# Kernel optimization log

Measured on AMD Instinct MI355X. Metric: run time of the kernel, lower is better.

The kernel has to match this reference:

```python
import jax, jax.numpy as jnp
import numpy as np

MAX_LEN = 200
MAX_K = 3
ITERATION = 3
NEG_PAD = -2.0 ** 16 + 1.0


def setup_inputs() -> dict:
    key = jax.random.key(0)
    k1, k2, k3, k4 = jax.random.split(key, 4)
    B, L, D_in, D_out = 1024, MAX_LEN, 128, 128
    low_capsule = jax.random.normal(k1, (B, L, D_in), dtype=jnp.float32)
    B_matrix = jax.random.normal(k2, (1, MAX_K, L), dtype=jnp.float32)
    S_matrix = jax.random.normal(k3, (D_in, D_out), dtype=jnp.float32)
    # lengths in [1, MAX_LEN]; at least one row hits MAX_LEN so max(seq_len)==MAX_LEN
    seq_len = jax.random.randint(k4, (B, 1), 1, MAX_LEN + 1, dtype=jnp.int64)
    seq_len = seq_len.at[0, 0].set(MAX_LEN)
    return {"low_capsule": low_capsule, "B_matrix": B_matrix,
            "S_matrix": S_matrix, "seq_len": seq_len}


def squash(x):
    # torch code: norm over dim=1 (the capsule axis), keepdim
    sq = jnp.sum(jnp.square(x), axis=1, keepdims=True)
    scale = sq / (1.0 + sq) / jnp.sqrt(sq + 1e-9)
    return scale * x


def reference(low_capsule, B_matrix, S_matrix, seq_len):
    # low_capsule: [B, L, D_in], B_matrix: [1, K, L], S_matrix: [D_in, D_out], seq_len: [B, 1]
    # mask: [B, K, L] (seq_len tiled over K via broadcasting)
    mask = jnp.arange(MAX_LEN)[None, None, :] < seq_len[:, :, None]
    # bilinear projection is loop-invariant (same math as recomputing each iter)
    low_new = jnp.einsum('bld,de->ble', low_capsule, S_matrix)  # [B, L, D_out]
    high = None
    for _ in range(ITERATION):
        logits = jnp.where(mask, B_matrix, jnp.float32(NEG_PAD))  # [B, K, L]
        W = jax.nn.softmax(logits, axis=-1)
        high = squash(jnp.einsum('bkl,ble->bke', W, low_new))  # [B, K, D_out]
        # agreement, summed over batch with keepdim -> [1, K, L]
        B_delta = jnp.einsum('bke,ble->kl', high, low_new)[None]
        B_matrix = B_matrix + B_delta
    return high
```

## Files before the change

### kernel.cpp

```cpp
#include <hip/hip_runtime.h>
#include <math.h>

#define BATCH 1024
#define SEQ   200
#define DIN   128
#define DOUT  128
#define HALF  64
#define PSTR  608

typedef __attribute__((ext_vector_type(8))) short short8;
typedef __attribute__((ext_vector_type(4))) float f32x4;

__device__ __forceinline__ void async_copy16(const void* g, void* l) {
    __builtin_amdgcn_global_load_lds((const __attribute__((address_space(1))) void*)g,
                                     (__attribute__((address_space(3))) void*)l,
                                     16, 0, 0);
}

__device__ __forceinline__ unsigned pack_split(float f) {
    unsigned u = __float_as_uint(f);
    unsigned r = u + 0x8000u;
    unsigned hi = r >> 16;
    float hf = __uint_as_float(r & 0xffff0000u);
    unsigned lo = __float_as_uint(f - hf) >> 16;
    return (hi << 16) | lo;
}

__device__ __forceinline__ void split2(float f, short& h, short& l) {
    unsigned u = __float_as_uint(f);
    unsigned r = u + 0x8000u;
    h = (short)(r >> 16);
    float hf = __uint_as_float(r & 0xffff0000u);
    l = (short)(__float_as_uint(f - hf) >> 16);
}

__device__ __forceinline__ float unpk(unsigned u) {
    return __uint_as_float(u & 0xffff0000u) + __uint_as_float(u << 16);
}

__global__ __launch_bounds__(256) void k_presplit(const float* __restrict__ S,
                                                  short* __restrict__ Sp) {
    int g = blockIdx.x * 256 + threadIdx.x;
    int j = g & 7, lane = (g >> 3) & 63, kt = (g >> 9) & 3, nt = g >> 11;
    int k = kt * 32 + (lane >> 4) * 8 + j;
    int n = nt * 16 + (lane & 15);
    short h, l;
    split2(S[k * DOUT + n], h, l);
    Sp[g] = h;
    Sp[16384 + g] = l;
}

__global__ __launch_bounds__(256, 2) void k_gemm(const float* __restrict__ A,
                                                 const short* __restrict__ Sp,
                                                 unsigned* __restrict__ outp) {
    __shared__ short sSp[32768];
    const int t = threadIdx.x;
    const int w = t >> 6, lane = t & 63;
    const int q = lane >> 4, c = lane & 15;
    const long rowb = (long)blockIdx.x * 128 + w * 32;

    float4 araw[4][2][2];
#pragma unroll
    for (int kt = 0; kt < 4; ++kt)
#pragma unroll
        for (int mt = 0; mt < 2; ++mt) {
            const float* ap = A + (rowb + mt * 16 + c) * DIN + kt * 32 + q * 8;
            araw[kt][mt][0] = *(const float4*)ap;
            araw[kt][mt][1] = *(const float4*)(ap + 4);
        }

#pragma unroll
    for (int i = 0; i < 16; ++i) {
        const int g = w * 16 + i;
        async_copy16(Sp + g * 512 + lane * 8, &sSp[g * 512]);
    }

    short8 ah[4][2], al[4][2];
#pragma unroll
    for (int kt = 0; kt < 4; ++kt)
#pragma unroll
        for (int mt = 0; mt < 2; ++mt) {
            float av[8];
            *(float4*)&av[0] = araw[kt][mt][0];
            *(float4*)&av[4] = araw[kt][mt][1];
#pragma unroll
            for (int j = 0; j < 8; ++j) {
                short h, l;
                split2(av[j], h, l);
                ah[kt][mt][j] = h; al[kt][mt][j] = l;
            }
        }

    f32x4 acc[2][8];
    const f32x4 zz = {0.f, 0.f, 0.f, 0.f};
#pragma unroll
    for (int mt = 0; mt < 2; ++mt)
#pragma unroll
        for (int nt = 0; nt < 8; ++nt) acc[mt][nt] = zz;

    __syncthreads();

#pragma unroll
    for (int kt = 0; kt < 4; ++kt)
#pragma unroll
        for (int nt = 0; nt < 8; ++nt) {
            const int fo = ((nt * 4 + kt) * 64 + lane) * 8;
            short8 sh = *(const short8*)&sSp[fo];
            short8 sl = *(const short8*)&sSp[16384 + fo];
#pragma unroll
            for (int mt = 0; mt < 2; ++mt) {
                acc[mt][nt] = __builtin_amdgcn_mfma_f32_16x16x32_bf16(ah[kt][mt], sh, acc[mt][nt], 0, 0, 0);
                acc[mt][nt] = __builtin_amdgcn_mfma_f32_16x16x32_bf16(al[kt][mt], sh, acc[mt][nt], 0, 0, 0);
                acc[mt][nt] = __builtin_amdgcn_mfma_f32_16x16x32_bf16(ah[kt][mt], sl, acc[mt][nt], 0, 0, 0);
            }
        }
#pragma unroll
    for (int mt = 0; mt < 2; ++mt)
#pragma unroll
        for (int nt = 0; nt < 8; ++nt) {
            long r0 = rowb + mt * 16 + q * 4;
#pragma unroll
            for (int r = 0; r < 4; ++r)
                outp[(r0 + r) * DOUT + nt * 16 + c] = pack_split(acc[mt][nt][r]);
        }
}

__global__ __launch_bounds__(256, 2) void k_iter(
    const unsigned* __restrict__ lowp,
    const float* __restrict__ Bm,
    const int* __restrict__ seq,
    const float* __restrict__ acc0, const float* __restrict__ acc1,
    float* __restrict__ part,
    float* __restrict__ out, int iter) {
    __shared__ unsigned sLn[SEQ * HALF];
    __shared__ float sW[SEQ * 4];
    __shared__ float pB[4][3][HALF];
    __shared__ float sH[3][HALF];

    const int t = threadIdx.x;
    const int lane = t & 63, w = t >> 6;
    const int b = blockIdx.x >> 1, half = blockIdx.x & 1;
    const unsigned* lp = lowp + (size_t)b * (SEQ * DIN) + half * HALF;
    const int n = seq[b];

    float a0v[4], a1v[4], a2v[4];
    if (w < 3) {
        const int k = w;
#pragma unroll
        for (int i = 0; i < 4; ++i) {
            int l = lane + 64 * i;
            bool inb = (l < SEQ);
            a0v[i] = inb ? Bm[k * SEQ + l] : 0.f;
            a1v[i] = (inb && iter >= 1) ? acc0[k * SEQ + l] : 0.f;
            a2v[i] = (inb && iter >= 2) ? acc1[k * SEQ + l] : 0.f;
        }
    }

    for (int g = w; g < 50; g += 4)
        async_copy16(lp + (g * 4 + (lane >> 4)) * DIN + (lane & 15) * 4,
                     &sLn[g * 256]);

    if (w < 3) {
        const int k = w;
        float vv[4], m = -INFINITY;
#pragma unroll
        for (int i = 0; i < 4; ++i) {
            int l = lane + 64 * i;
            float v = a0v[i] + a1v[i] + a2v[i];
            vv[i] = (l < n) ? v : -INFINITY;
            if (l < n) m = fmaxf(m, v);
        }
        for (int off = 32; off; off >>= 1) m = fmaxf(m, __shfl_xor(m, off, 64));
        float s = 0.f, pv[4];
#pragma unroll
        for (int i = 0; i < 4; ++i) {
            pv[i] = (vv[i] == -INFINITY) ? 0.f : expf(vv[i] - m);
            s += pv[i];
        }
        for (int off = 32; off; off >>= 1) s += __shfl_xor(s, off, 64);
        float rs = 1.f / s;
#pragma unroll
        for (int i = 0; i < 4; ++i) {
            int l = lane + 64 * i;
            if (l < SEQ) sW[l * 4 + k] = pv[i] * rs;
        }
    }
    __syncthreads();

    {
        const int e = lane;
        float h0 = 0.f, h1 = 0.f, h2 = 0.f;
        for (int i = 0; i < 50; ++i) {
            int l = w * 50 + i;
            float4 wv = *(const float4*)&sW[l * 4];
            float f = unpk(sLn[l * 64 + e]);
            h0 = fmaf(wv.x, f, h0);
            h1 = fmaf(wv.y, f, h1);
            h2 = fmaf(wv.z, f, h2);
        }
        pB[w][0][e] = h0; pB[w][1][e] = h1; pB[w][2][e] = h2;
    }
    __syncthreads();

    if (t < HALF) {
        float g0 = pB[0][0][t] + pB[1][0][t] + pB[2][0][t] + pB[3][0][t];
        float g1 = pB[0][1][t] + pB[1][1][t] + pB[2][1][t] + pB[3][1][t];
        float g2 = pB[0][2][t] + pB[1][2][t] + pB[2][2][t] + pB[3][2][t];
        float sq = g0 * g0 + g1 * g1 + g2 * g2;
        float scale = sq / (1.f + sq) / sqrtf(sq + 1e-9f);
        g0 *= scale; g1 *= scale; g2 *= scale;
        if (iter == 2) {
            size_t o = (size_t)b * 3 * DOUT + half * HALF + t;
            out[o] = g0; out[o + DOUT] = g1; out[o + 2 * DOUT] = g2;
        } else {
            sH[0][t] = g0; sH[1][t] = g1; sH[2][t] = g2;
        }
    }
    if (iter == 2) return;
    __syncthreads();

    if (t < SEQ) {
        const int l = t;
        float d0 = 0.f, d1 = 0.f, d2 = 0.f;
#pragma unroll
        for (int j = 0; j < 16; ++j) {
            const int jj = (j + l) & 15;
            uint4 u = *(const uint4*)&sLn[l * 64 + 4 * jj];
            float4 x0 = *(const float4*)&sH[0][4 * jj];
            float4 x1 = *(const float4*)&sH[1][4 * jj];
            float4 x2 = *(const float4*)&sH[2][4 * jj];
            float f0 = unpk(u.x), f1 = unpk(u.y), f2 = unpk(u.z), f3 = unpk(u.w);
            d0 += x0.x * f0 + x0.y * f1 + x0.z * f2 + x0.w * f3;
            d1 += x1.x * f0 + x1.y * f1 + x1.z * f2 + x1.w * f3;
            d2 += x2.x * f0 + x2.y * f1 + x2.z * f2 + x2.w * f3;
        }
        float* pp = part + (size_t)blockIdx.x * PSTR;
        pp[l] = d0;
        pp[SEQ + l] = d1;
        pp[2 * SEQ + l] = d2;
    }
}

__global__ __launch_bounds__(256) void k_reduce(const float* __restrict__ part,
                                                float* __restrict__ accN) {
    __shared__ float sP[4][4];
    const int t = threadIdx.x, lane = t & 63, w = t >> 6;
    const int c4 = blockIdx.x * 4;
    float sx = 0.f, sy = 0.f, sz = 0.f, sw = 0.f;
#pragma unroll
    for (int i = 0; i < 8; ++i) {
        float4 v = *(const float4*)&part[(size_t)(t + 256 * i) * PSTR + c4];
        sx += v.x; sy += v.y; sz += v.z; sw += v.w;
    }
#pragma unroll
    for (int off = 1; off < 64; off <<= 1) {
        sx += __shfl_xor(sx, off, 64);
        sy += __shfl_xor(sy, off, 64);
        sz += __shfl_xor(sz, off, 64);
        sw += __shfl_xor(sw, off, 64);
    }
    if (lane == 0) { sP[w][0] = sx; sP[w][1] = sy; sP[w][2] = sz; sP[w][3] = sw; }
    __syncthreads();
    if (t < 4)
        accN[c4 + t] = sP[0][t] + sP[1][t] + sP[2][t] + sP[3][t];
}

extern "C" void kernel_launch(void* const* d_in, const int* in_sizes, int n_in,
                              void* d_out, int out_size, void* d_ws, size_t ws_size,
                              hipStream_t stream) {
    const float* low_capsule = (const float*)d_in[0];
    const float* B_matrix    = (const float*)d_in[1];
    const float* S_matrix    = (const float*)d_in[2];
    const int*   seq_len     = (const int*)d_in[3];
    float* out = (float*)d_out;

    unsigned* lowp = (unsigned*)d_ws;
    short* Sp      = (short*)(lowp + (size_t)BATCH * SEQ * DOUT);
    float* acc0    = (float*)(Sp + 32768);
    float* acc1    = acc0 + 640;
    float* part    = acc1 + 640;

    k_presplit<<<64, 256, 0, stream>>>(S_matrix, Sp);
    k_gemm<<<(BATCH * SEQ) / 128, 256, 0, stream>>>(low_capsule, Sp, lowp);

    k_iter<<<2 * BATCH, 256, 0, stream>>>(lowp, B_matrix, seq_len, acc0, acc1, part, out, 0);
    k_reduce<<<150, 256, 0, stream>>>(part, acc0);
    k_iter<<<2 * BATCH, 256, 0, stream>>>(lowp, B_matrix, seq_len, acc0, acc1, part, out, 1);
    k_reduce<<<150, 256, 0, stream>>>(part, acc1);
    k_iter<<<2 * BATCH, 256, 0, stream>>>(lowp, B_matrix, seq_len, acc0, acc1, part, out, 2);
}
```

Baseline: 284.8 us.

## Persistent double-buffered GEMM, quarter-width iter blocks with prefetch, atomic reduce

```diff
diff --git a/kernel.cpp b/kernel.cpp
--- a/kernel.cpp
+++ b/kernel.cpp
@@ -5,7 +5,7 @@
 #define SEQ   200
 #define DIN   128
 #define DOUT  128
-#define HALF  64
+#define GSTR  260
 #define PSTR  608
 
 typedef __attribute__((ext_vector_type(8))) short short8;
@@ -57,72 +57,75 @@
     const int t = threadIdx.x;
     const int w = t >> 6, lane = t & 63;
     const int q = lane >> 4, c = lane & 15;
-    const long rowb = (long)blockIdx.x * 128 + w * 32;
-
-    float4 araw[4][2][2];
-#pragma unroll
-    for (int kt = 0; kt < 4; ++kt)
-#pragma unroll
-        for (int mt = 0; mt < 2; ++mt) {
-            const float* ap = A + (rowb + mt * 16 + c) * DIN + kt * 32 + q * 8;
-            araw[kt][mt][0] = *(const float4*)ap;
-            araw[kt][mt][1] = *(const float4*)(ap + 4);
-        }
-
+    const int GD = gridDim.x;
+    const int NT = (BATCH * SEQ) / 64;
+
+    float4 bA[8], bB[8];
+
+    auto PF = [&](int tile, float4* buf) {
+        const float* ap = A + ((long)tile * 64 + w * 16 + c) * DIN + q * 8;
+#pragma unroll
+        for (int kt = 0; kt < 4; ++kt) {
+            buf[2 * kt]     = *(const float4*)(ap + kt * 32);
+            buf[2 * kt + 1] = *(const float4*)(ap + kt * 32 + 4);
+        }
+    };
+    auto COMPUTE = [&](int tile, const float4* buf) {
+        short8 ah[4], al[4];
+#pragma unroll
+        for (int kt = 0; kt < 4; ++kt) {
+            float av[8];
+            *(float4*)&av[0] = buf[2 * kt];
+            *(float4*)&av[4] = buf[2 * kt + 1];
+#pragma unroll
+            for (int j = 0; j < 8; ++j) {
+                short h, l;
+                split2(av[j], h, l);
+                ah[kt][j] = h; al[kt][j] = l;
+            }
+        }
+        f32x4 acc[8];
+        const f32x4 zz = {0.f, 0.f, 0.f, 0.f};
+#pragma unroll
+        for (int nt = 0; nt < 8; ++nt) acc[nt] = zz;
+#pragma unroll
+        for (int kt = 0; kt < 4; ++kt)
+#pragma unroll
+            for (int nt = 0; nt < 8; ++nt) {
+                const int fo = ((nt * 4 + kt) * 64 + lane) * 8;
+                short8 sh = *(const short8*)&sSp[fo];
+                short8 sl = *(const short8*)&sSp[16384 + fo];
+                acc[nt] = __builtin_amdgcn_mfma_f32_16x16x32_bf16(ah[kt], sh, acc[nt], 0, 0, 0);
+                acc[nt] = __builtin_amdgcn_mfma_f32_16x16x32_bf16(al[kt], sh, acc[nt], 0, 0, 0);
+                acc[nt] = __builtin_amdgcn_mfma_f32_16x16x32_bf16(ah[kt], sl, acc[nt], 0, 0, 0);
+            }
+        const long r0 = (long)tile * 64 + w * 16 + q * 4;
+#pragma unroll
+        for (int nt = 0; nt < 8; ++nt)
+#pragma unroll
+            for (int r = 0; r < 4; ++r)
+                outp[(r0 + r) * DOUT + nt * 16 + c] = pack_split(acc[nt][r]);
+    };
+
+    int ti = blockIdx.x;
+    PF(ti, bA);
 #pragma unroll
     for (int i = 0; i < 16; ++i) {
         const int g = w * 16 + i;
         async_copy16(Sp + g * 512 + lane * 8, &sSp[g * 512]);
     }
-
-    short8 ah[4][2], al[4][2];
-#pragma unroll
-    for (int kt = 0; kt < 4; ++kt)
-#pragma unroll
-        for (int mt = 0; mt < 2; ++mt) {
-            float av[8];
-            *(float4*)&av[0] = araw[kt][mt][0];
-            *(float4*)&av[4] = araw[kt][mt][1];
-#pragma unroll
-            for (int j = 0; j < 8; ++j) {
-                short h, l;
-                split2(av[j], h, l);
-                ah[kt][mt][j] = h; al[kt][mt][j] = l;
-            }
-        }
-
-    f32x4 acc[2][8];
-    const f32x4 zz = {0.f, 0.f, 0.f, 0.f};
-#pragma unroll
-    for (int mt = 0; mt < 2; ++mt)
-#pragma unroll
-        for (int nt = 0; nt < 8; ++nt) acc[mt][nt] = zz;
-
     __syncthreads();
-
-#pragma unroll
-    for (int kt = 0; kt < 4; ++kt)
-#pragma unroll
-        for (int nt = 0; nt < 8; ++nt) {
-            const int fo = ((nt * 4 + kt) * 64 + lane) * 8;
-            short8 sh = *(const short8*)&sSp[fo];
-            short8 sl = *(const short8*)&sSp[16384 + fo];
-#pragma unroll
-            for (int mt = 0; mt < 2; ++mt) {
-                acc[mt][nt] = __builtin_amdgcn_mfma_f32_16x16x32_bf16(ah[kt][mt], sh, acc[mt][nt], 0, 0, 0);
-                acc[mt][nt] = __builtin_amdgcn_mfma_f32_16x16x32_bf16(al[kt][mt], sh, acc[mt][nt], 0, 0, 0);
-                acc[mt][nt] = __builtin_amdgcn_mfma_f32_16x16x32_bf16(ah[kt][mt], sl, acc[mt][nt], 0, 0, 0);
-            }
-        }
-#pragma unroll
-    for (int mt = 0; mt < 2; ++mt)
-#pragma unroll
-        for (int nt = 0; nt < 8; ++nt) {
-            long r0 = rowb + mt * 16 + q * 4;
-#pragma unroll
-            for (int r = 0; r < 4; ++r)
-                outp[(r0 + r) * DOUT + nt * 16 + c] = pack_split(acc[mt][nt][r]);
-        }
+    int tn = ti + GD;
+    for (;;) {
+        if (tn < NT) PF(tn, bB);
+        COMPUTE(ti, bA);
+        ti = tn; tn += GD;
+        if (ti >= NT) break;
+        if (tn < NT) PF(tn, bA);
+        COMPUTE(ti, bB);
+        ti = tn; tn += GD;
+        if (ti >= NT) break;
+    }
 }
 
 __global__ __launch_bounds__(256, 2) void k_iter(
@@ -132,137 +135,142 @@
     const float* __restrict__ acc0, const float* __restrict__ acc1,
     float* __restrict__ part,
     float* __restrict__ out, int iter) {
-    __shared__ unsigned sLn[SEQ * HALF];
+    __shared__ unsigned sLn[2][25 * GSTR];
     __shared__ float sW[SEQ * 4];
-    __shared__ float pB[4][3][HALF];
-    __shared__ float sH[3][HALF];
-
-    const int t = threadIdx.x;
-    const int lane = t & 63, w = t >> 6;
-    const int b = blockIdx.x >> 1, half = blockIdx.x & 1;
-    const unsigned* lp = lowp + (size_t)b * (SEQ * DIN) + half * HALF;
-    const int n = seq[b];
-
-    float a0v[4], a1v[4], a2v[4];
-    if (w < 3) {
-        const int k = w;
-#pragma unroll
-        for (int i = 0; i < 4; ++i) {
-            int l = lane + 64 * i;
-            bool inb = (l < SEQ);
-            a0v[i] = inb ? Bm[k * SEQ + l] : 0.f;
-            a1v[i] = (inb && iter >= 1) ? acc0[k * SEQ + l] : 0.f;
-            a2v[i] = (inb && iter >= 2) ? acc1[k * SEQ + l] : 0.f;
-        }
-    }
-
-    for (int g = w; g < 50; g += 4)
-        async_copy16(lp + (g * 4 + (lane >> 4)) * DIN + (lane & 15) * 4,
-                     &sLn[g * 256]);
-
-    if (w < 3) {
-        const int k = w;
-        float vv[4], m = -INFINITY;
-#pragma unroll
-        for (int i = 0; i < 4; ++i) {
-            int l = lane + 64 * i;
-            float v = a0v[i] + a1v[i] + a2v[i];
-            vv[i] = (l < n) ? v : -INFINITY;
-            if (l < n) m = fmaxf(m, v);
-        }
-        for (int off = 32; off; off >>= 1) m = fmaxf(m, __shfl_xor(m, off, 64));
-        float s = 0.f, pv[4];
-#pragma unroll
-        for (int i = 0; i < 4; ++i) {
-            pv[i] = (vv[i] == -INFINITY) ? 0.f : expf(vv[i] - m);
-            s += pv[i];
-        }
-        for (int off = 32; off; off >>= 1) s += __shfl_xor(s, off, 64);
-        float rs = 1.f / s;
-#pragma unroll
-        for (int i = 0; i < 4; ++i) {
-            int l = lane + 64 * i;
-            if (l < SEQ) sW[l * 4 + k] = pv[i] * rs;
-        }
-    }
+    __shared__ float pB[4][3][32];
+    __shared__ float sH[3][32];
+
+    const int t = threadIdx.x, lane = t & 63, w = t >> 6;
+
+    float r0[4], r1[4], r2[4];
+    auto RAW = [&](int b) {
+        if (w < 3) {
+#pragma unroll
+            for (int i = 0; i < 4; ++i) {
+                int l = lane + 64 * i; bool inb = l < SEQ;
+                r0[i] = inb ? Bm[w * SEQ + l] : 0.f;
+                r1[i] = (inb && iter >= 1) ? acc0[w * SEQ + l] : 0.f;
+                r2[i] = (inb && iter >= 2) ? acc1[w * SEQ + l] : 0.f;
+            }
+        }
+    };
+    auto STAGE = [&](int b, int qr, unsigned* sb) {
+        const unsigned* lp = lowp + (size_t)b * (SEQ * DIN) + qr * 32;
+        for (int g = w; g < 25; g += 4)
+            async_copy16(lp + (g * 8 + (lane >> 3)) * DIN + (lane & 7) * 4,
+                         &sb[g * GSTR]);
+    };
+    auto FIN = [&](int b) {
+        if (w < 3) {
+            const int n = seq[b];
+            float m = -INFINITY, vv[4];
+#pragma unroll
+            for (int i = 0; i < 4; ++i) {
+                int l = lane + 64 * i;
+                float v = r0[i] + r1[i] + r2[i];
+                vv[i] = (l < n) ? v : -INFINITY;
+                if (l < n) m = fmaxf(m, v);
+            }
+            for (int off = 32; off; off >>= 1) m = fmaxf(m, __shfl_xor(m, off, 64));
+            float s = 0.f, pv[4];
+#pragma unroll
+            for (int i = 0; i < 4; ++i) {
+                pv[i] = (vv[i] == -INFINITY) ? 0.f : expf(vv[i] - m);
+                s += pv[i];
+            }
+            for (int off = 32; off; off >>= 1) s += __shfl_xor(s, off, 64);
+            float rs = 1.f / s;
+#pragma unroll
+            for (int i = 0; i < 4; ++i) {
+                int l = lane + 64 * i;
+                if (l < SEQ) sW[l * 4 + w] = pv[i] * rs;
+            }
+        }
+    };
+    auto CORE_BH = [&](const unsigned* sb, int b, int qr) {
+        const int el = t & 31, lg = t >> 5;
+        float h0 = 0.f, h1 = 0.f, h2 = 0.f;
+#pragma unroll
+        for (int i = 0; i < 25; ++i) {
+            int l = lg * 25 + i;
+            float4 wv = *(const float4*)&sW[l * 4];
+            float f = unpk(sb[(l >> 3) * GSTR + (l & 7) * 32 + el]);
+            h0 = fmaf(wv.x, f, h0); h1 = fmaf(wv.y, f, h1); h2 = fmaf(wv.z, f, h2);
+        }
+        h0 += __shfl_xor(h0, 32, 64);
+        h1 += __shfl_xor(h1, 32, 64);
+        h2 += __shfl_xor(h2, 32, 64);
+        if (lane < 32) { pB[w][0][el] = h0; pB[w][1][el] = h1; pB[w][2][el] = h2; }
+        __syncthreads();
+        if (t < 32) {
+            float g0 = pB[0][0][t] + pB[1][0][t] + pB[2][0][t] + pB[3][0][t];
+            float g1 = pB[0][1][t] + pB[1][1][t] + pB[2][1][t] + pB[3][1][t];
+            float g2 = pB[0][2][t] + pB[1][2][t] + pB[2][2][t] + pB[3][2][t];
+            float sq = g0 * g0 + g1 * g1 + g2 * g2;
+            float scale = sq / (1.f + sq) / sqrtf(sq + 1e-9f);
+            g0 *= scale; g1 *= scale; g2 *= scale;
+            if (iter == 2) {
+                size_t o = (size_t)b * 3 * DOUT + qr * 32 + t;
+                out[o] = g0; out[o + DOUT] = g1; out[o + 2 * DOUT] = g2;
+            } else { sH[0][t] = g0; sH[1][t] = g1; sH[2][t] = g2; }
+        }
+        __syncthreads();
+    };
+    auto CORE_C = [&](const unsigned* sb, int tau) {
+        if (iter == 2) return;
+        if (t < SEQ) {
+            const int l = t;
+            float d0 = 0.f, d1 = 0.f, d2 = 0.f;
+#pragma unroll
+            for (int j = 0; j < 8; ++j) {
+                const int jj = (j + (l & 7) + (l >> 3)) & 7;
+                uint4 u = *(const uint4*)&sb[(l >> 3) * GSTR + (l & 7) * 32 + 4 * jj];
+                float4 x0 = *(const float4*)&sH[0][4 * jj];
+                float4 x1 = *(const float4*)&sH[1][4 * jj];
+                float4 x2 = *(const float4*)&sH[2][4 * jj];
+                float f0 = unpk(u.x), f1 = unpk(u.y), f2 = unpk(u.z), f3 = unpk(u.w);
+                d0 += x0.x * f0 + x0.y * f1 + x0.z * f2 + x0.w * f3;
+                d1 += x1.x * f0 + x1.y * f1 + x1.z * f2 + x1.w * f3;
+                d2 += x2.x * f0 + x2.y * f1 + x2.z * f2 + x2.w * f3;
+            }
+            float* pp = part + (size_t)tau * PSTR;
+            pp[l] = d0; pp[SEQ + l] = d1; pp[2 * SEQ + l] = d2;
+        }
+    };
+
+    const int tau0 = blockIdx.x, tau1 = blockIdx.x + 2048;
+    const int b0 = tau0 >> 2, q0 = tau0 & 3;
+    const int b1 = tau1 >> 2, q1 = tau1 & 3;
+
+    RAW(b0);
+    STAGE(b0, q0, sLn[0]);
+    FIN(b0);
     __syncthreads();
-
-    {
-        const int e = lane;
-        float h0 = 0.f, h1 = 0.f, h2 = 0.f;
-        for (int i = 0; i < 50; ++i) {
-            int l = w * 50 + i;
-            float4 wv = *(const float4*)&sW[l * 4];
-            float f = unpk(sLn[l * 64 + e]);
-            h0 = fmaf(wv.x, f, h0);
-            h1 = fmaf(wv.y, f, h1);
-            h2 = fmaf(wv.z, f, h2);
-        }
-        pB[w][0][e] = h0; pB[w][1][e] = h1; pB[w][2][e] = h2;
-    }
+    CORE_BH(sLn[0], b0, q0);
+    RAW(b1);
+    STAGE(b1, q1, sLn[1]);
+    CORE_C(sLn[0], tau0);
+    FIN(b1);
     __syncthreads();
-
-    if (t < HALF) {
-        float g0 = pB[0][0][t] + pB[1][0][t] + pB[2][0][t] + pB[3][0][t];
-        float g1 = pB[0][1][t] + pB[1][1][t] + pB[2][1][t] + pB[3][1][t];
-        float g2 = pB[0][2][t] + pB[1][2][t] + pB[2][2][t] + pB[3][2][t];
-        float sq = g0 * g0 + g1 * g1 + g2 * g2;
-        float scale = sq / (1.f + sq) / sqrtf(sq + 1e-9f);
-        g0 *= scale; g1 *= scale; g2 *= scale;
-        if (iter == 2) {
-            size_t o = (size_t)b * 3 * DOUT + half * HALF + t;
-            out[o] = g0; out[o + DOUT] = g1; out[o + 2 * DOUT] = g2;
-        } else {
-            sH[0][t] = g0; sH[1][t] = g1; sH[2][t] = g2;
-        }
-    }
-    if (iter == 2) return;
-    __syncthreads();
-
-    if (t < SEQ) {
-        const int l = t;
-        float d0 = 0.f, d1 = 0.f, d2 = 0.f;
-#pragma unroll
-        for (int j = 0; j < 16; ++j) {
-            const int jj = (j + l) & 15;
-            uint4 u = *(const uint4*)&sLn[l * 64 + 4 * jj];
-            float4 x0 = *(const float4*)&sH[0][4 * jj];
-            float4 x1 = *(const float4*)&sH[1][4 * jj];
-            float4 x2 = *(const float4*)&sH[2][4 * jj];
-            float f0 = unpk(u.x), f1 = unpk(u.y), f2 = unpk(u.z), f3 = unpk(u.w);
-            d0 += x0.x * f0 + x0.y * f1 + x0.z * f2 + x0.w * f3;
-            d1 += x1.x * f0 + x1.y * f1 + x1.z * f2 + x1.w * f3;
-            d2 += x2.x * f0 + x2.y * f1 + x2.z * f2 + x2.w * f3;
-        }
-        float* pp = part + (size_t)blockIdx.x * PSTR;
-        pp[l] = d0;
-        pp[SEQ + l] = d1;
-        pp[2 * SEQ + l] = d2;
-    }
+    CORE_BH(sLn[1], b1, q1);
+    CORE_C(sLn[1], tau1);
 }
 
 __global__ __launch_bounds__(256) void k_reduce(const float* __restrict__ part,
                                                 float* __restrict__ accN) {
-    __shared__ float sP[4][4];
-    const int t = threadIdx.x, lane = t & 63, w = t >> 6;
-    const int c4 = blockIdx.x * 4;
-    float sx = 0.f, sy = 0.f, sz = 0.f, sw = 0.f;
-#pragma unroll
-    for (int i = 0; i < 8; ++i) {
-        float4 v = *(const float4*)&part[(size_t)(t + 256 * i) * PSTR + c4];
-        sx += v.x; sy += v.y; sz += v.z; sw += v.w;
+    const int t = threadIdx.x;
+    const int r0 = blockIdx.x * 32;
+    if (t < 150) {
+        float sx = 0.f, sy = 0.f, sz = 0.f, sw = 0.f;
+        for (int r = 0; r < 32; ++r) {
+            float4 v = *(const float4*)&part[(size_t)(r0 + r) * PSTR + t * 4];
+            sx += v.x; sy += v.y; sz += v.z; sw += v.w;
+        }
+        atomicAdd(&accN[4 * t + 0], sx);
+        atomicAdd(&accN[4 * t + 1], sy);
+        atomicAdd(&accN[4 * t + 2], sz);
+        atomicAdd(&accN[4 * t + 3], sw);
     }
-#pragma unroll
-    for (int off = 1; off < 64; off <<= 1) {
-        sx += __shfl_xor(sx, off, 64);
-        sy += __shfl_xor(sy, off, 64);
-        sz += __shfl_xor(sz, off, 64);
-        sw += __shfl_xor(sw, off, 64);
-    }
-    if (lane == 0) { sP[w][0] = sx; sP[w][1] = sy; sP[w][2] = sz; sP[w][3] = sw; }
-    __syncthreads();
-    if (t < 4)
-        accN[c4 + t] = sP[0][t] + sP[1][t] + sP[2][t] + sP[3][t];
 }
 
 extern "C" void kernel_launch(void* const* d_in, const int* in_sizes, int n_in,
@@ -280,12 +288,14 @@
     float* acc1    = acc0 + 640;
     float* part    = acc1 + 640;
 
+    hipMemsetAsync(acc0, 0, 1280 * sizeof(float), stream);
+
     k_presplit<<<64, 256, 0, stream>>>(S_matrix, Sp);
-    k_gemm<<<(BATCH * SEQ) / 128, 256, 0, stream>>>(low_capsule, Sp, lowp);
-
-    k_iter<<<2 * BATCH, 256, 0, stream>>>(lowp, B_matrix, seq_len, acc0, acc1, part, out, 0);
-    k_reduce<<<150, 256, 0, stream>>>(part, acc0);
-    k_iter<<<2 * BATCH, 256, 0, stream>>>(lowp, B_matrix, seq_len, acc0, acc1, part, out, 1);
-    k_reduce<<<150, 256, 0, stream>>>(part, acc1);
-    k_iter<<<2 * BATCH, 256, 0, stream>>>(lowp, B_matrix, seq_len, acc0, acc1, part, out, 2);
-}
+    k_gemm<<<512, 256, 0, stream>>>(low_capsule, Sp, lowp);
+
+    k_iter<<<2048, 256, 0, stream>>>(lowp, B_matrix, seq_len, acc0, acc1, part, out, 0);
+    k_reduce<<<128, 256, 0, stream>>>(part, acc0);
+    k_iter<<<2048, 256, 0, stream>>>(lowp, B_matrix, seq_len, acc0, acc1, part, out, 1);
+    k_reduce<<<128, 256, 0, stream>>>(part, acc1);
+    k_iter<<<2048, 256, 0, stream>>>(lowp, B_matrix, seq_len, acc0, acc1, part, out, 2);
+}
```

Result: slower. 371.8 us (+30.5%).
